# Performance work log

Measured on AMD Instinct MI355X. Metric: run time of the kernel, lower is better.

The kernel has to match this reference:

```python
import jax, jax.numpy as jnp
import numpy as np


def _spectral_normalize(W):
    # spectral_norm divides the weight by its largest singular value
    sigma = jnp.linalg.norm(W, ord=2)
    return W / sigma


def setup_inputs() -> dict:
    key = jax.random.key(0)
    ks = jax.random.split(key, 8)
    B, C, H, W = 2, 64, 96, 96
    C8 = C // 8
    x = jax.random.normal(ks[0], (B, C, H, W), dtype=jnp.float32)
    Wq = jax.random.normal(ks[1], (C8, C), dtype=jnp.float32) * 0.1
    bq = jax.random.normal(ks[2], (C8,), dtype=jnp.float32) * 0.1
    Wk = jax.random.normal(ks[3], (C8, C), dtype=jnp.float32) * 0.1
    bk = jax.random.normal(ks[4], (C8,), dtype=jnp.float32) * 0.1
    Wv = jax.random.normal(ks[5], (C, C), dtype=jnp.float32) * 0.1
    bv = jax.random.normal(ks[6], (C,), dtype=jnp.float32) * 0.1
    gamma = jnp.ones((1,), dtype=jnp.float32)
    return {"x": x, "Wq": Wq, "bq": bq, "Wk": Wk, "bk": bk,
            "Wv": Wv, "bv": bv, "gamma": gamma}


def reference(x, Wq, bq, Wk, bk, Wv, bv, gamma):
    B, C, H, W = x.shape
    xf = x.reshape(B, C, H * W)                       # [B, C, N]
    Wq_n = _spectral_normalize(Wq)
    Wk_n = _spectral_normalize(Wk)
    Wv_n = _spectral_normalize(Wv)
    # 1x1 Conv1d == matmul over channel dim
    f = jnp.einsum('oc,bcn->bon', Wq_n, xf) + bq[None, :, None]   # [B, C/8, N]
    g = jnp.einsum('oc,bcn->bon', Wk_n, xf) + bk[None, :, None]   # [B, C/8, N]
    h = jnp.einsum('oc,bcn->bon', Wv_n, xf) + bv[None, :, None]   # [B, C, N]
    # scores[b,i,j] = sum_c f[b,c,i] * g[b,c,j];  softmax over dim=1 (i)
    scores = jnp.einsum('bci,bcj->bij', f, g)                      # [B, N, N]
    beta = jax.nn.softmax(scores, axis=1)
    # o[b,c,j] = sum_i h[b,c,i] * beta[b,i,j]
    o = gamma[0] * jnp.einsum('bci,bij->bcj', h, beta) + xf
    return o.reshape(B, C, H, W)
```

## Files before the change

### kernel.cpp

```cpp
#include <hip/hip_runtime.h>


#define N_PIX 9216
#define N_B   2
#define N_C   64

typedef _Float16 half8  __attribute__((ext_vector_type(8)));
typedef _Float16 half4v __attribute__((ext_vector_type(4)));
typedef float    float4v __attribute__((ext_vector_type(4)));

#define LOG2E 1.44269504088896340736f
#define EXP_SHIFT 12.0f

__global__ __launch_bounds__(64) void k_sigma(const float* __restrict__ Wq,
                                              const float* __restrict__ Wk,
                                              const float* __restrict__ Wv,
                                              float* __restrict__ sig) {
  __shared__ float G8[8][8];
  __shared__ float Wl[64 * 64];
  __shared__ _Float16 Wh[64 * 80];
  __shared__ _Float16 Gh[64 * 80];
  const int t = threadIdx.x;
  const int mat = blockIdx.x;
  if (mat < 2) {
    const float* W = (mat == 0) ? Wq : Wk;
    const int i = t >> 3, j = t & 7;
    float g = 0.f;
    for (int c = 0; c < 64; ++c) g += W[i * 64 + c] * W[j * 64 + c];
    G8[i][j] = g;
    __syncthreads();
    const int L = t & 7;
    float G0[8], Gr[8];
    for (int k = 0; k < 8; ++k) { G0[k] = G8[L][k]; Gr[k] = G0[k]; }
    for (int it = 0; it < 8; ++it) {
      float g2[8] = {0, 0, 0, 0, 0, 0, 0, 0};
      for (int k = 0; k < 8; ++k) {
        float gik = Gr[k];
        for (int jj = 0; jj < 8; ++jj) g2[jj] += gik * __shfl(Gr[jj], k, 64);
      }
      float mx = 0.f;
      for (int jj = 0; jj < 8; ++jj) mx = fmaxf(mx, fabsf(g2[jj]));
      for (int d = 1; d < 8; d <<= 1) mx = fmaxf(mx, __shfl_xor(mx, d, 64));
      float r = 1.f / mx;
      for (int jj = 0; jj < 8; ++jj) Gr[jj] = g2[jj] * r;
    }
    float u = 0.f;
    for (int jj = 0; jj < 8; ++jj) u += Gr[jj];
    float y = 0.f;
    for (int k = 0; k < 8; ++k) y += G0[k] * __shfl(u, k, 64);
    float nu = u * y, de = u * u;
    for (int d = 1; d < 8; d <<= 1) { nu += __shfl_xor(nu, d, 64); de += __shfl_xor(de, d, 64); }
    if (t == 0) sig[mat] = sqrtf(nu / de);
  } else {
    for (int idx = t; idx < 4096; idx += 64) Wl[idx] = Wv[idx];
    __syncthreads();
    for (int idx = t; idx < 4096; idx += 64) Wh[(idx >> 6) * 80 + (idx & 63)] = (_Float16)Wl[idx];
    __syncthreads();
    const int lane15 = t & 15, quad = t >> 4;
    half8 fr[4][2];
    for (int rb = 0; rb < 4; ++rb)
      for (int kc = 0; kc < 2; ++kc)
        fr[rb][kc] = *(const half8*)&Wh[(lane15 + 16 * rb) * 80 + 32 * kc + 8 * quad];
    float4v D[4][4];
    for (int mb = 0; mb < 4; ++mb) for (int nb = 0; nb < 4; ++nb) D[mb][nb] = (float4v){0.f, 0.f, 0.f, 0.f};
    for (int kc = 0; kc < 2; ++kc)
      for (int mb = 0; mb < 4; ++mb)
        for (int nb = 0; nb < 4; ++nb)
          D[mb][nb] = __builtin_amdgcn_mfma_f32_16x16x32_f16(fr[mb][kc], fr[nb][kc], D[mb][nb], 0, 0, 0);
    for (int it = 0; it < 8; ++it) {
      float mx = 0.f;
      for (int mb = 0; mb < 4; ++mb) for (int nb = 0; nb < 4; ++nb) for (int r = 0; r < 4; ++r)
        mx = fmaxf(mx, fabsf(D[mb][nb][r]));
      for (int d = 1; d < 64; d <<= 1) mx = fmaxf(mx, __shfl_xor(mx, d, 64));
      float rs = 1.f / mx;
      for (int mb = 0; mb < 4; ++mb) for (int nb = 0; nb < 4; ++nb) for (int r = 0; r < 4; ++r)
        Gh[(4 * quad + r + 16 * mb) * 80 + lane15 + 16 * nb] = (_Float16)(D[mb][nb][r] * rs);
      __syncthreads();
      if (it == 7) break;
      for (int rb = 0; rb < 4; ++rb)
        for (int kc = 0; kc < 2; ++kc)
          fr[rb][kc] = *(const half8*)&Gh[(lane15 + 16 * rb) * 80 + 32 * kc + 8 * quad];
      for (int mb = 0; mb < 4; ++mb) for (int nb = 0; nb < 4; ++nb) D[mb][nb] = (float4v){0.f, 0.f, 0.f, 0.f};
      for (int kc = 0; kc < 2; ++kc)
        for (int mb = 0; mb < 4; ++mb)
          for (int nb = 0; nb < 4; ++nb)
            D[mb][nb] = __builtin_amdgcn_mfma_f32_16x16x32_f16(fr[mb][kc], fr[nb][kc], D[mb][nb], 0, 0, 0);
      __syncthreads();
    }
    float u = 0.f;
    for (int c = 0; c < 64; ++c) u += (float)Gh[t * 80 + c];
    float z = 0.f;
    for (int i2 = 0; i2 < 64; ++i2) z += Wl[i2 * 64 + t] * __shfl(u, i2, 64);
    float nu = z * z, de = u * u;
    for (int d = 1; d < 64; d <<= 1) { nu += __shfl_xor(nu, d, 64); de += __shfl_xor(de, d, 64); }
    if (t == 0) sig[2] = sqrtf(nu / de);
  }
}

__global__ __launch_bounds__(128) void k_wconv(const float* __restrict__ Wq, const float* __restrict__ bq,
                                               const float* __restrict__ Wk, const float* __restrict__ bk,
                                               const float* __restrict__ Wv, const float* __restrict__ bv,
                                               const float* __restrict__ sig,
                                               _Float16* __restrict__ W16, float* __restrict__ b80,
                                               unsigned* __restrict__ maxKu) {
  const float iq = LOG2E / sig[0], ik = 1.0f / sig[1], iv = 1.0f / sig[2];
  const int t = threadIdx.x;
  for (int idx = t; idx < 80 * 64; idx += 128) {
    const int m = idx >> 6, c = idx & 63;
    float v;
    if (m < 8)       v = Wq[m * 64 + c] * iq;
    else if (m < 16) v = Wk[(m - 8) * 64 + c] * ik;
    else             v = Wv[(m - 16) * 64 + c] * iv;
    W16[idx] = (_Float16)v;
  }
  if (t < 80) {
    float v;
    if (t < 8)       v = bq[t] * LOG2E;
    else if (t < 16) v = bk[t - 8];
    else             v = bv[t - 16];
    b80[t] = v;
  }
  if (t < 2) maxKu[t] = 0u;
}

__global__ __launch_bounds__(256) void k_fgh(const float* __restrict__ x,
                                             const _Float16* __restrict__ W16,
                                             const float* __restrict__ b80,
                                             _Float16* __restrict__ K16,
                                             _Float16* __restrict__ Q16,
                                             _Float16* __restrict__ VT16,
                                             unsigned* __restrict__ maxKu) {
  const int wave = threadIdx.x >> 6;
  const int lane = threadIdx.x & 63;
  const int lane15 = lane & 15, quad = lane >> 4;
  const int tile = blockIdx.x * 4 + wave;
  const int b = tile / 576;
  const int n = (tile % 576) * 16 + lane15;
  half8 wf[5][2];
  for (int mb = 0; mb < 5; ++mb)
    for (int kc = 0; kc < 2; ++kc)
      wf[mb][kc] = *(const half8*)&W16[(lane15 + 16 * mb) * 64 + 32 * kc + 8 * quad];
  float4v acc[5];
  for (int mb = 0; mb < 5; ++mb) acc[mb] = *(const float4v*)&b80[16 * mb + 4 * quad];
  const float* xb = x + (size_t)b * N_C * N_PIX;
  for (int kc = 0; kc < 2; ++kc) {
    half8 bf;
    for (int j = 0; j < 8; ++j)
      bf[j] = (_Float16)xb[(size_t)(32 * kc + 8 * quad + j) * N_PIX + n];
    for (int mb = 0; mb < 5; ++mb)
      acc[mb] = __builtin_amdgcn_mfma_f32_16x16x32_f16(wf[mb][kc], bf, acc[mb], 0, 0, 0);
  }
  {
    _Float16* dstK = K16 + ((size_t)b * N_PIX + n) * 8;
    _Float16* dstQ = Q16 + ((size_t)b * N_PIX + n) * 8;
    for (int r = 0; r < 4; ++r) {
      const int m = 4 * quad + r;
      const _Float16 v = (_Float16)acc[0][r];
      if (m < 8) dstK[m] = v; else dstQ[m - 8] = v;
    }
  }
  for (int mb = 1; mb < 5; ++mb)
    for (int r = 0; r < 4; ++r) {
      const int c = 4 * quad + r + 16 * (mb - 1);
      VT16[((size_t)b * N_C + c) * N_PIX + n] = (_Float16)acc[mb][r];
    }
  float sq = 0.f;
  if (quad < 2)
    for (int r = 0; r < 4; ++r) sq += acc[0][r] * acc[0][r];
  sq += __shfl_xor(sq, 16, 64);
  for (int d = 1; d < 64; d <<= 1) sq = fmaxf(sq, __shfl_xor(sq, d, 64));
  if (lane == 0) atomicMax(&maxKu[b], __float_as_uint(sq));
}


__device__ __forceinline__ void gload16(const _Float16* g, _Float16* l) {
  __builtin_amdgcn_global_load_lds(
      (const __attribute__((address_space(1))) void*)g,
      (__attribute__((address_space(3))) void*)l, 16, 0, 0);
}

__global__ __launch_bounds__(256, 2) void k_attn(const _Float16* __restrict__ K16,
                                                 const _Float16* __restrict__ Q16,
                                                 const _Float16* __restrict__ VT16,
                                                 const unsigned* __restrict__ maxKu,
                                                 const float* __restrict__ x,
                                                 const float* __restrict__ gamma,
                                                 float* __restrict__ out) {
  __shared__ __align__(16) _Float16 Vld[2][64 * 64];
  __shared__ __align__(16) _Float16 Pld[2][32 * 72];
  __shared__ float Lsh[4][32];
  const int wave = threadIdx.x >> 6;
  const int lane = threadIdx.x & 63;
  const int lane15 = lane & 15, quad = lane >> 4;
  const int tile = blockIdx.x;
  const int b = tile / 288;
  const int jb = (tile % 288) * 32;
  const float gm = gamma[0];
  const _Float16* Kb = K16 + (size_t)b * N_PIX * 8;
  const _Float16* Vb = VT16 + (size_t)b * N_C * N_PIX;
  const int srow = lane >> 3;
  const int scol = (lane & 7) ^ srow;
  const _Float16* gV0 = Vb + (size_t)(16 * wave + srow) * N_PIX + scol * 8;
  const _Float16* gV1 = Vb + (size_t)(16 * wave + 8 + srow) * N_PIX + scol * 8;

  half8 qf0 = {}, qf1 = {};
  if (quad == 0) {
    qf0 = *(const half8*)(Q16 + ((size_t)b * N_PIX + jb + lane15) * 8);
    qf1 = *(const half8*)(Q16 + ((size_t)b * N_PIX + jb + 16 + lane15) * 8);
  }
  const float maxK = sqrtf(__uint_as_float(maxKu[b]));
  float nq0 = 0.f, nq1 = 0.f;
  if (quad == 0)
#pragma unroll
    for (int j = 0; j < 8; ++j) {
      nq0 += (float)qf0[j] * (float)qf0[j];
      nq1 += (float)qf1[j] * (float)qf1[j];
    }
  nq0 = __shfl(nq0, lane15, 64);
  nq1 = __shfl(nq1, lane15, 64);
  const float M0 = sqrtf(nq0) * maxK - EXP_SHIFT;
  const float M1 = sqrtf(nq1) * maxK - EXP_SHIFT;

  float4v acc0 = {0.f, 0.f, 0.f, 0.f}, acc1 = {0.f, 0.f, 0.f, 0.f};
  float ls0 = 0.f, ls1 = 0.f;
  half8 kA = {}, kB = {};

  gload16(gV0, &Vld[0][(16 * wave) * 64]);
  gload16(gV1, &Vld[0][(16 * wave + 8) * 64]);
  if (quad == 0) kA = *(const half8*)(Kb + (size_t)(16 * wave + lane15) * 8);

  const float4v f4z = {0.f, 0.f, 0.f, 0.f};
#define ROUND(I0, BUF, KF, KN, PREF)                                                       \
  {                                                                                        \
    const int i1 = (I0) + 64;                                                              \
    if (PREF) {                                                                            \
      gload16(gV0 + i1, &Vld[BUF ^ 1][(16 * wave) * 64]);                                  \
      gload16(gV1 + i1, &Vld[BUF ^ 1][(16 * wave + 8) * 64]);                              \
      if (quad == 0) KN = *(const half8*)(Kb + (size_t)(i1 + 16 * wave + lane15) * 8);     \
    }                                                                                      \
    float4v s0 = __builtin_amdgcn_mfma_f32_16x16x32_f16(KF, qf0, f4z, 0, 0, 0);            \
    float4v s1 = __builtin_amdgcn_mfma_f32_16x16x32_f16(KF, qf1, f4z, 0, 0, 0);            \
    half4v h0, h1;                                                                         \
    _Pragma("unroll") for (int r = 0; r < 4; ++r) {                                        \
      const float p0 = __builtin_amdgcn_exp2f(s0[r] - M0);                                 \
      const float p1 = __builtin_amdgcn_exp2f(s1[r] - M1);                                 \
      h0[r] = (_Float16)p0; ls0 += (float)h0[r];                                           \
      h1[r] = (_Float16)p1; ls1 += (float)h1[r];                                           \
    }                                                                                      \
    *(half4v*)&Pld[BUF][lane15 * 72 + 16 * wave + 4 * quad] = h0;                          \
    *(half4v*)&Pld[BUF][(16 + lane15) * 72 + 16 * wave + 4 * quad] = h1;                   \
    __syncthreads();                                                                       \
    const half8 pf00 = *(const half8*)&Pld[BUF][lane15 * 72 + 8 * quad];                   \
    const half8 pf01 = *(const half8*)&Pld[BUF][lane15 * 72 + 32 + 8 * quad];              \
    const half8 pf10 = *(const half8*)&Pld[BUF][(16 + lane15) * 72 + 8 * quad];            \
    const half8 pf11 = *(const half8*)&Pld[BUF][(16 + lane15) * 72 + 32 + 8 * quad];       \
    const half8 vf0 = *(const half8*)&Vld[BUF][(16 * wave + lane15) * 64 +                 \
                                              ((quad ^ (lane15 & 7)) << 3)];               \
    const half8 vf1 = *(const half8*)&Vld[BUF][(16 * wave + lane15) * 64 +                 \
                                              (((4 + quad) ^ (lane15 & 7)) << 3)];         \
    acc0 = __builtin_amdgcn_mfma_f32_16x16x32_f16(pf00, vf0, acc0, 0, 0, 0);               \
    acc0 = __builtin_amdgcn_mfma_f32_16x16x32_f16(pf01, vf1, acc0, 0, 0, 0);               \
    acc1 = __builtin_amdgcn_mfma_f32_16x16x32_f16(pf10, vf0, acc1, 0, 0, 0);               \
    acc1 = __builtin_amdgcn_mfma_f32_16x16x32_f16(pf11, vf1, acc1, 0, 0, 0);               \
  }

#pragma unroll 1
  for (int r2 = 0; r2 < N_PIX / 128; ++r2) {
    const int i0 = r2 * 128;
    ROUND(i0, 0, kA, kB, true)
    ROUND(i0 + 64, 1, kB, kA, (i0 + 128) < N_PIX)
  }
#undef ROUND

  ls0 += __shfl_xor(ls0, 16, 64); ls0 += __shfl_xor(ls0, 32, 64);
  ls1 += __shfl_xor(ls1, 16, 64); ls1 += __shfl_xor(ls1, 32, 64);
  if (quad == 0) { Lsh[wave][lane15] = ls0; Lsh[wave][16 + lane15] = ls1; }
  __syncthreads();
  float4v lt0 = {0.f, 0.f, 0.f, 0.f}, lt1 = {0.f, 0.f, 0.f, 0.f};
#pragma unroll
  for (int w = 0; w < 4; ++w) {
    const float4v a = *(const float4v*)&Lsh[w][4 * quad];
    const float4v c = *(const float4v*)&Lsh[w][16 + 4 * quad];
#pragma unroll
    for (int r = 0; r < 4; ++r) { lt0[r] += a[r]; lt1[r] += c[r]; }
  }
  const int ch = 16 * wave + lane15;
  const float* xb = x + (size_t)b * N_C * N_PIX;
  float* ob = out + (size_t)b * N_C * N_PIX;
  {
    const size_t idx = (size_t)ch * N_PIX + jb + 4 * quad;
    const float4v xr = *(const float4v*)(xb + idx);
    float4v o;
#pragma unroll
    for (int r = 0; r < 4; ++r) o[r] = gm * acc0[r] / lt0[r] + xr[r];
    *(float4v*)(ob + idx) = o;
  }
  {
    const size_t idx = (size_t)ch * N_PIX + jb + 16 + 4 * quad;
    const float4v xr = *(const float4v*)(xb + idx);
    float4v o;
#pragma unroll
    for (int r = 0; r < 4; ++r) o[r] = gm * acc1[r] / lt1[r] + xr[r];
    *(float4v*)(ob + idx) = o;
  }
}

extern "C" void kernel_launch(void* const* d_in, const int* in_sizes, int n_in,
                              void* d_out, int out_size, void* d_ws, size_t ws_size,
                              hipStream_t stream) {
  const float* x     = (const float*)d_in[0];
  const float* Wq    = (const float*)d_in[1];
  const float* bq    = (const float*)d_in[2];
  const float* Wk    = (const float*)d_in[3];
  const float* bk    = (const float*)d_in[4];
  const float* Wv    = (const float*)d_in[5];
  const float* bv    = (const float*)d_in[6];
  const float* gamma = (const float*)d_in[7];
  float* out = (float*)d_out;

  char* ws = (char*)d_ws;
  float*    sig   = (float*)ws;
  unsigned* maxKu = (unsigned*)(ws + 16);
  float*    b80   = (float*)(ws + 32);
  _Float16* W16   = (_Float16*)(ws + 512);
  _Float16* K16   = (_Float16*)(ws + 10752);
  _Float16* Q16   = (_Float16*)(ws + 10752 + 294912);
  _Float16* VT16  = (_Float16*)(ws + 10752 + 2 * 294912);

  hipLaunchKernelGGL(k_sigma, dim3(3), dim3(64), 0, stream, Wq, Wk, Wv, sig);
  hipLaunchKernelGGL(k_wconv, dim3(1), dim3(128), 0, stream, Wq, bq, Wk, bk, Wv, bv, sig, W16, b80, maxKu);
  hipLaunchKernelGGL(k_fgh, dim3(288), dim3(256), 0, stream, x, W16, b80, K16, Q16, VT16, maxKu);
  hipLaunchKernelGGL(k_attn, dim3(576), dim3(256), 0, stream, K16, Q16, VT16, maxKu, x, gamma, out);
}
```

Measured before the change: 200.8 us.

## Split key range across waves with private P tiles and final cross-wave reduction

Each wave now handles its own interleaved slice of the key/pixel dimension and computes all 64 output channels for the 32 query columns. This removes the per-round __syncthreads and the shared V staging. V fragments are loaded straight from global memory into registers, double-buffered in registers. Partial outputs are reduced across the four waves through a new shared Osh buffer at the end. The trade-off is higher register pressure (eight accumulators plus eight V fragments) and uncoalesced 16-byte global V loads per lane, with no LDS reuse of V across waves.

```diff
diff --git a/kernel.cpp b/kernel.cpp
--- a/kernel.cpp
+++ b/kernel.cpp
@@ -173,12 +173,6 @@
 }
 
 
-__device__ __forceinline__ void gload16(const _Float16* g, _Float16* l) {
-  __builtin_amdgcn_global_load_lds(
-      (const __attribute__((address_space(1))) void*)g,
-      (__attribute__((address_space(3))) void*)l, 16, 0, 0);
-}
-
 __global__ __launch_bounds__(256, 2) void k_attn(const _Float16* __restrict__ K16,
                                                  const _Float16* __restrict__ Q16,
                                                  const _Float16* __restrict__ VT16,
@@ -186,9 +180,9 @@
                                                  const float* __restrict__ x,
                                                  const float* __restrict__ gamma,
                                                  float* __restrict__ out) {
-  __shared__ __align__(16) _Float16 Vld[2][64 * 64];
-  __shared__ __align__(16) _Float16 Pld[2][32 * 72];
+  __shared__ __align__(16) _Float16 P_lds[4][32 * 40];
   __shared__ float Lsh[4][32];
+  __shared__ float Osh[4][64][33];
   const int wave = threadIdx.x >> 6;
   const int lane = threadIdx.x & 63;
   const int lane15 = lane & 15, quad = lane >> 4;
@@ -198,10 +192,11 @@
   const float gm = gamma[0];
   const _Float16* Kb = K16 + (size_t)b * N_PIX * 8;
   const _Float16* Vb = VT16 + (size_t)b * N_C * N_PIX;
-  const int srow = lane >> 3;
-  const int scol = (lane & 7) ^ srow;
-  const _Float16* gV0 = Vb + (size_t)(16 * wave + srow) * N_PIX + scol * 8;
-  const _Float16* gV1 = Vb + (size_t)(16 * wave + 8 + srow) * N_PIX + scol * 8;
+  _Float16* Pl = P_lds[wave];
+  const _Float16* pV0 = Vb + (size_t)(lane15) * N_PIX + 8 * quad;
+  const _Float16* pV1 = Vb + (size_t)(lane15 + 16) * N_PIX + 8 * quad;
+  const _Float16* pV2 = Vb + (size_t)(lane15 + 32) * N_PIX + 8 * quad;
+  const _Float16* pV3 = Vb + (size_t)(lane15 + 48) * N_PIX + 8 * quad;
 
   half8 qf0 = {}, qf1 = {};
   if (quad == 0) {
@@ -221,60 +216,87 @@
   const float M0 = sqrtf(nq0) * maxK - EXP_SHIFT;
   const float M1 = sqrtf(nq1) * maxK - EXP_SHIFT;
 
-  float4v acc0 = {0.f, 0.f, 0.f, 0.f}, acc1 = {0.f, 0.f, 0.f, 0.f};
+  float4v a00 = {0.f,0.f,0.f,0.f}, a01 = {0.f,0.f,0.f,0.f}, a02 = {0.f,0.f,0.f,0.f}, a03 = {0.f,0.f,0.f,0.f};
+  float4v a10 = {0.f,0.f,0.f,0.f}, a11 = {0.f,0.f,0.f,0.f}, a12 = {0.f,0.f,0.f,0.f}, a13 = {0.f,0.f,0.f,0.f};
   float ls0 = 0.f, ls1 = 0.f;
-  half8 kA = {}, kB = {};
-
-  gload16(gV0, &Vld[0][(16 * wave) * 64]);
-  gload16(gV1, &Vld[0][(16 * wave + 8) * 64]);
-  if (quad == 0) kA = *(const half8*)(Kb + (size_t)(16 * wave + lane15) * 8);
-
   const float4v f4z = {0.f, 0.f, 0.f, 0.f};
-#define ROUND(I0, BUF, KF, KN, PREF)                                                       \
-  {                                                                                        \
-    const int i1 = (I0) + 64;                                                              \
-    if (PREF) {                                                                            \
-      gload16(gV0 + i1, &Vld[BUF ^ 1][(16 * wave) * 64]);                                  \
-      gload16(gV1 + i1, &Vld[BUF ^ 1][(16 * wave + 8) * 64]);                              \
-      if (quad == 0) KN = *(const half8*)(Kb + (size_t)(i1 + 16 * wave + lane15) * 8);     \
-    }                                                                                      \
-    float4v s0 = __builtin_amdgcn_mfma_f32_16x16x32_f16(KF, qf0, f4z, 0, 0, 0);            \
-    float4v s1 = __builtin_amdgcn_mfma_f32_16x16x32_f16(KF, qf1, f4z, 0, 0, 0);            \
-    half4v h0, h1;                                                                         \
-    _Pragma("unroll") for (int r = 0; r < 4; ++r) {                                        \
-      const float p0 = __builtin_amdgcn_exp2f(s0[r] - M0);                                 \
-      const float p1 = __builtin_amdgcn_exp2f(s1[r] - M1);                                 \
-      h0[r] = (_Float16)p0; ls0 += (float)h0[r];                                           \
-      h1[r] = (_Float16)p1; ls1 += (float)h1[r];                                           \
-    }                                                                                      \
-    *(half4v*)&Pld[BUF][lane15 * 72 + 16 * wave + 4 * quad] = h0;                          \
-    *(half4v*)&Pld[BUF][(16 + lane15) * 72 + 16 * wave + 4 * quad] = h1;                   \
-    __syncthreads();                                                                       \
-    const half8 pf00 = *(const half8*)&Pld[BUF][lane15 * 72 + 8 * quad];                   \
-    const half8 pf01 = *(const half8*)&Pld[BUF][lane15 * 72 + 32 + 8 * quad];              \
-    const half8 pf10 = *(const half8*)&Pld[BUF][(16 + lane15) * 72 + 8 * quad];            \
-    const half8 pf11 = *(const half8*)&Pld[BUF][(16 + lane15) * 72 + 32 + 8 * quad];       \
-    const half8 vf0 = *(const half8*)&Vld[BUF][(16 * wave + lane15) * 64 +                 \
-                                              ((quad ^ (lane15 & 7)) << 3)];               \
-    const half8 vf1 = *(const half8*)&Vld[BUF][(16 * wave + lane15) * 64 +                 \
-                                              (((4 + quad) ^ (lane15 & 7)) << 3)];         \
-    acc0 = __builtin_amdgcn_mfma_f32_16x16x32_f16(pf00, vf0, acc0, 0, 0, 0);               \
-    acc0 = __builtin_amdgcn_mfma_f32_16x16x32_f16(pf01, vf1, acc0, 0, 0, 0);               \
-    acc1 = __builtin_amdgcn_mfma_f32_16x16x32_f16(pf10, vf0, acc1, 0, 0, 0);               \
-    acc1 = __builtin_amdgcn_mfma_f32_16x16x32_f16(pf11, vf1, acc1, 0, 0, 0);               \
+
+  half8 kA0 = {}, kA1 = {}, kB0 = {}, kB1 = {};
+  half8 vA0, vA1, vA2, vA3, vB0, vB1, vB2, vB3;
+
+#define LOADK(K0, K1, I)                                                \
+  if (quad == 0) {                                                      \
+    K0 = *(const half8*)(Kb + (size_t)((I) + lane15) * 8);              \
+    K1 = *(const half8*)(Kb + (size_t)((I) + 16 + lane15) * 8);         \
+  }
+#define LOADV(V0, V1, V2, V3, I)                                        \
+  V0 = *(const half8*)(pV0 + (I));                                      \
+  V1 = *(const half8*)(pV1 + (I));                                      \
+  V2 = *(const half8*)(pV2 + (I));                                      \
+  V3 = *(const half8*)(pV3 + (I));
+
+  const int base = 32 * wave;
+  LOADK(kA0, kA1, base)
+  LOADV(vA0, vA1, vA2, vA3, base)
+
+#define ROUND(KF0, KF1, VF0, VF1, VF2, VF3, KN0, KN1, VN0, VN1, VN2, VN3, PI, PREF) \
+  {                                                                                 \
+    if (PREF) { LOADK(KN0, KN1, PI) LOADV(VN0, VN1, VN2, VN3, PI) }                 \
+    float4v s00 = __builtin_amdgcn_mfma_f32_16x16x32_f16(KF0, qf0, f4z, 0, 0, 0);   \
+    float4v s01 = __builtin_amdgcn_mfma_f32_16x16x32_f16(KF0, qf1, f4z, 0, 0, 0);   \
+    float4v s10 = __builtin_amdgcn_mfma_f32_16x16x32_f16(KF1, qf0, f4z, 0, 0, 0);   \
+    float4v s11 = __builtin_amdgcn_mfma_f32_16x16x32_f16(KF1, qf1, f4z, 0, 0, 0);   \
+    half4v h00, h01, h10, h11;                                                      \
+    _Pragma("unroll") for (int r = 0; r < 4; ++r) {                                 \
+      const float p00 = __builtin_amdgcn_exp2f(s00[r] - M0);                        \
+      const float p01 = __builtin_amdgcn_exp2f(s01[r] - M1);                        \
+      const float p10 = __builtin_amdgcn_exp2f(s10[r] - M0);                        \
+      const float p11 = __builtin_amdgcn_exp2f(s11[r] - M1);                        \
+      h00[r] = (_Float16)p00; ls0 += (float)h00[r];                                 \
+      h01[r] = (_Float16)p01; ls1 += (float)h01[r];                                 \
+      h10[r] = (_Float16)p10; ls0 += (float)h10[r];                                 \
+      h11[r] = (_Float16)p11; ls1 += (float)h11[r];                                 \
+    }                                                                               \
+    *(half4v*)&Pl[lane15 * 40 + 4 * quad] = h00;                                    \
+    *(half4v*)&Pl[lane15 * 40 + 16 + 4 * quad] = h10;                               \
+    *(half4v*)&Pl[(16 + lane15) * 40 + 4 * quad] = h01;                             \
+    *(half4v*)&Pl[(16 + lane15) * 40 + 16 + 4 * quad] = h11;                        \
+    const half8 pf0 = *(const half8*)&Pl[lane15 * 40 + 8 * quad];                   \
+    const half8 pf1 = *(const half8*)&Pl[(16 + lane15) * 40 + 8 * quad];            \
+    a00 = __builtin_amdgcn_mfma_f32_16x16x32_f16(pf0, VF0, a00, 0, 0, 0);           \
+    a01 = __builtin_amdgcn_mfma_f32_16x16x32_f16(pf0, VF1, a01, 0, 0, 0);           \
+    a02 = __builtin_amdgcn_mfma_f32_16x16x32_f16(pf0, VF2, a02, 0, 0, 0);           \
+    a03 = __builtin_amdgcn_mfma_f32_16x16x32_f16(pf0, VF3, a03, 0, 0, 0);           \
+    a10 = __builtin_amdgcn_mfma_f32_16x16x32_f16(pf1, VF0, a10, 0, 0, 0);           \
+    a11 = __builtin_amdgcn_mfma_f32_16x16x32_f16(pf1, VF1, a11, 0, 0, 0);           \
+    a12 = __builtin_amdgcn_mfma_f32_16x16x32_f16(pf1, VF2, a12, 0, 0, 0);           \
+    a13 = __builtin_amdgcn_mfma_f32_16x16x32_f16(pf1, VF3, a13, 0, 0, 0);           \
   }
 
 #pragma unroll 1
-  for (int r2 = 0; r2 < N_PIX / 128; ++r2) {
-    const int i0 = r2 * 128;
-    ROUND(i0, 0, kA, kB, true)
-    ROUND(i0 + 64, 1, kB, kA, (i0 + 128) < N_PIX)
+  for (int j = 0; j < 36; ++j) {
+    const int i0 = 256 * j + base;
+    ROUND(kA0, kA1, vA0, vA1, vA2, vA3, kB0, kB1, vB0, vB1, vB2, vB3, i0 + 128, true)
+    ROUND(kB0, kB1, vB0, vB1, vB2, vB3, kA0, kA1, vA0, vA1, vA2, vA3, i0 + 256, j < 35)
   }
 #undef ROUND
+#undef LOADK
+#undef LOADV
 
   ls0 += __shfl_xor(ls0, 16, 64); ls0 += __shfl_xor(ls0, 32, 64);
   ls1 += __shfl_xor(ls1, 16, 64); ls1 += __shfl_xor(ls1, 32, 64);
   if (quad == 0) { Lsh[wave][lane15] = ls0; Lsh[wave][16 + lane15] = ls1; }
+#pragma unroll
+  for (int r = 0; r < 4; ++r) {
+    Osh[wave][lane][r]      = a00[r];
+    Osh[wave][lane][4 + r]  = a01[r];
+    Osh[wave][lane][8 + r]  = a02[r];
+    Osh[wave][lane][12 + r] = a03[r];
+    Osh[wave][lane][16 + r] = a10[r];
+    Osh[wave][lane][20 + r] = a11[r];
+    Osh[wave][lane][24 + r] = a12[r];
+    Osh[wave][lane][28 + r] = a13[r];
+  }
   __syncthreads();
   float4v lt0 = {0.f, 0.f, 0.f, 0.f}, lt1 = {0.f, 0.f, 0.f, 0.f};
 #pragma unroll
@@ -284,6 +306,14 @@
 #pragma unroll
     for (int r = 0; r < 4; ++r) { lt0[r] += a[r]; lt1[r] += c[r]; }
   }
+  float4v o0 = {0.f, 0.f, 0.f, 0.f}, o1 = {0.f, 0.f, 0.f, 0.f};
+#pragma unroll
+  for (int w = 0; w < 4; ++w)
+#pragma unroll
+    for (int r = 0; r < 4; ++r) {
+      o0[r] += Osh[w][lane][4 * wave + r];
+      o1[r] += Osh[w][lane][16 + 4 * wave + r];
+    }
   const int ch = 16 * wave + lane15;
   const float* xb = x + (size_t)b * N_C * N_PIX;
   float* ob = out + (size_t)b * N_C * N_PIX;
@@ -292,7 +322,7 @@
     const float4v xr = *(const float4v*)(xb + idx);
     float4v o;
 #pragma unroll
-    for (int r = 0; r < 4; ++r) o[r] = gm * acc0[r] / lt0[r] + xr[r];
+    for (int r = 0; r < 4; ++r) o[r] = gm * o0[r] / lt0[r] + xr[r];
     *(float4v*)(ob + idx) = o;
   }
   {
@@ -300,7 +330,7 @@
     const float4v xr = *(const float4v*)(xb + idx);
     float4v o;
 #pragma unroll
-    for (int r = 0; r < 4; ++r) o[r] = gm * acc1[r] / lt1[r] + xr[r];
+    for (int r = 0; r < 4; ++r) o[r] = gm * o1[r] / lt1[r] + xr[r];
     *(float4v*)(ob + idx) = o;
   }
 }
```

Measured after the change: 221.0 us. 10.0% more time.

## Split key range across waves to remove per-round block barriers in attention

Applied to the files above, without the earlier changes.

Each wave now handles its own 32-key slice per round for all 64 channels, keeping per-wave K/V/P tiles in LDS. This removes the __syncthreads per round. Partial output accumulators are reduced across waves through shared memory at the end. LDS reads and vmcnt waits use inline asm to control the pipelining. The cost is more accumulator registers (8 MFMA tiles) and an extra LDS reduction epilogue.

```diff
diff --git a/kernel.cpp b/kernel.cpp
--- a/kernel.cpp
+++ b/kernel.cpp
@@ -8,6 +8,7 @@
 typedef _Float16 half8  __attribute__((ext_vector_type(8)));
 typedef _Float16 half4v __attribute__((ext_vector_type(4)));
 typedef float    float4v __attribute__((ext_vector_type(4)));
+typedef int      int4v  __attribute__((ext_vector_type(4)));
 
 #define LOG2E 1.44269504088896340736f
 #define EXP_SHIFT 12.0f
@@ -179,6 +180,22 @@
       (__attribute__((address_space(3))) void*)l, 16, 0, 0);
 }
 
+#define VMWAIT5() asm volatile("s_waitcnt vmcnt(5)" ::: "memory")
+#define DS2(D0, D1, P0, P1)                                              \
+  asm volatile("ds_read_b128 %0, %2\n\t"                                 \
+               "ds_read_b128 %1, %3\n\t"                                 \
+               "s_waitcnt lgkmcnt(0)"                                    \
+               : "=&v"(D0), "=&v"(D1) : "v"(P0), "v"(P1) : "memory")
+#define DS4(D0, D1, D2, D3, P0, P1, P2, P3)                              \
+  asm volatile("ds_read_b128 %0, %4\n\t"                                 \
+               "ds_read_b128 %1, %5\n\t"                                 \
+               "ds_read_b128 %2, %6\n\t"                                 \
+               "ds_read_b128 %3, %7\n\t"                                 \
+               "s_waitcnt lgkmcnt(0)"                                    \
+               : "=&v"(D0), "=&v"(D1), "=&v"(D2), "=&v"(D3)              \
+               : "v"(P0), "v"(P1), "v"(P2), "v"(P3) : "memory")
+typedef const __attribute__((address_space(3))) _Float16* lds_cp;
+
 __global__ __launch_bounds__(256, 2) void k_attn(const _Float16* __restrict__ K16,
                                                  const _Float16* __restrict__ Q16,
                                                  const _Float16* __restrict__ VT16,
@@ -186,9 +203,11 @@
                                                  const float* __restrict__ x,
                                                  const float* __restrict__ gamma,
                                                  float* __restrict__ out) {
-  __shared__ __align__(16) _Float16 Vld[2][64 * 64];
-  __shared__ __align__(16) _Float16 Pld[2][32 * 72];
+  __shared__ __align__(16) _Float16 Kld[2][4][64 * 8];
+  __shared__ __align__(16) _Float16 Vld[2][4][64 * 32];
+  __shared__ __align__(16) _Float16 Pld[4][32 * 40];
   __shared__ float Lsh[4][32];
+  __shared__ float Osh[4][64][17];
   const int wave = threadIdx.x >> 6;
   const int lane = threadIdx.x & 63;
   const int lane15 = lane & 15, quad = lane >> 4;
@@ -198,10 +217,7 @@
   const float gm = gamma[0];
   const _Float16* Kb = K16 + (size_t)b * N_PIX * 8;
   const _Float16* Vb = VT16 + (size_t)b * N_C * N_PIX;
-  const int srow = lane >> 3;
-  const int scol = (lane & 7) ^ srow;
-  const _Float16* gV0 = Vb + (size_t)(16 * wave + srow) * N_PIX + scol * 8;
-  const _Float16* gV1 = Vb + (size_t)(16 * wave + 8 + srow) * N_PIX + scol * 8;
+  _Float16* Pl = Pld[wave];
 
   half8 qf0 = {}, qf1 = {};
   if (quad == 0) {
@@ -221,60 +237,93 @@
   const float M0 = sqrtf(nq0) * maxK - EXP_SHIFT;
   const float M1 = sqrtf(nq1) * maxK - EXP_SHIFT;
 
-  float4v acc0 = {0.f, 0.f, 0.f, 0.f}, acc1 = {0.f, 0.f, 0.f, 0.f};
+  float4v a00 = {0.f,0.f,0.f,0.f}, a01 = {0.f,0.f,0.f,0.f}, a02 = {0.f,0.f,0.f,0.f}, a03 = {0.f,0.f,0.f,0.f};
+  float4v a10 = {0.f,0.f,0.f,0.f}, a11 = {0.f,0.f,0.f,0.f}, a12 = {0.f,0.f,0.f,0.f}, a13 = {0.f,0.f,0.f,0.f};
   float ls0 = 0.f, ls1 = 0.f;
-  half8 kA = {}, kB = {};
-
-  gload16(gV0, &Vld[0][(16 * wave) * 64]);
-  gload16(gV1, &Vld[0][(16 * wave + 8) * 64]);
-  if (quad == 0) kA = *(const half8*)(Kb + (size_t)(16 * wave + lane15) * 8);
-
   const float4v f4z = {0.f, 0.f, 0.f, 0.f};
-#define ROUND(I0, BUF, KF, KN, PREF)                                                       \
-  {                                                                                        \
-    const int i1 = (I0) + 64;                                                              \
-    if (PREF) {                                                                            \
-      gload16(gV0 + i1, &Vld[BUF ^ 1][(16 * wave) * 64]);                                  \
-      gload16(gV1 + i1, &Vld[BUF ^ 1][(16 * wave + 8) * 64]);                              \
-      if (quad == 0) KN = *(const half8*)(Kb + (size_t)(i1 + 16 * wave + lane15) * 8);     \
-    }                                                                                      \
-    float4v s0 = __builtin_amdgcn_mfma_f32_16x16x32_f16(KF, qf0, f4z, 0, 0, 0);            \
-    float4v s1 = __builtin_amdgcn_mfma_f32_16x16x32_f16(KF, qf1, f4z, 0, 0, 0);            \
-    half4v h0, h1;                                                                         \
-    _Pragma("unroll") for (int r = 0; r < 4; ++r) {                                        \
-      const float p0 = __builtin_amdgcn_exp2f(s0[r] - M0);                                 \
-      const float p1 = __builtin_amdgcn_exp2f(s1[r] - M1);                                 \
-      h0[r] = (_Float16)p0; ls0 += (float)h0[r];                                           \
-      h1[r] = (_Float16)p1; ls1 += (float)h1[r];                                           \
-    }                                                                                      \
-    *(half4v*)&Pld[BUF][lane15 * 72 + 16 * wave + 4 * quad] = h0;                          \
-    *(half4v*)&Pld[BUF][(16 + lane15) * 72 + 16 * wave + 4 * quad] = h1;                   \
-    __syncthreads();                                                                       \
-    const half8 pf00 = *(const half8*)&Pld[BUF][lane15 * 72 + 8 * quad];                   \
-    const half8 pf01 = *(const half8*)&Pld[BUF][lane15 * 72 + 32 + 8 * quad];              \
-    const half8 pf10 = *(const half8*)&Pld[BUF][(16 + lane15) * 72 + 8 * quad];            \
-    const half8 pf11 = *(const half8*)&Pld[BUF][(16 + lane15) * 72 + 32 + 8 * quad];       \
-    const half8 vf0 = *(const half8*)&Vld[BUF][(16 * wave + lane15) * 64 +                 \
-                                              ((quad ^ (lane15 & 7)) << 3)];               \
-    const half8 vf1 = *(const half8*)&Vld[BUF][(16 * wave + lane15) * 64 +                 \
-                                              (((4 + quad) ^ (lane15 & 7)) << 3)];         \
-    acc0 = __builtin_amdgcn_mfma_f32_16x16x32_f16(pf00, vf0, acc0, 0, 0, 0);               \
-    acc0 = __builtin_amdgcn_mfma_f32_16x16x32_f16(pf01, vf1, acc0, 0, 0, 0);               \
-    acc1 = __builtin_amdgcn_mfma_f32_16x16x32_f16(pf10, vf0, acc1, 0, 0, 0);               \
-    acc1 = __builtin_amdgcn_mfma_f32_16x16x32_f16(pf11, vf1, acc1, 0, 0, 0);               \
-  }
+
+#define STAGE(SLOT, I0)                                                          \
+  {                                                                              \
+    const int _i = (I0);                                                         \
+    gload16(Kb + (size_t)(_i + (lane & 31)) * 8, &Kld[SLOT][wave][0]);           \
+    gload16(Vb + (size_t)(lane >> 2) * N_PIX + _i + (lane & 3) * 8,              \
+            &Vld[SLOT][wave][0]);                                                \
+    gload16(Vb + (size_t)(16 + (lane >> 2)) * N_PIX + _i + (lane & 3) * 8,       \
+            &Vld[SLOT][wave][512]);                                              \
+    gload16(Vb + (size_t)(32 + (lane >> 2)) * N_PIX + _i + (lane & 3) * 8,       \
+            &Vld[SLOT][wave][1024]);                                             \
+    gload16(Vb + (size_t)(48 + (lane >> 2)) * N_PIX + _i + (lane & 3) * 8,       \
+            &Vld[SLOT][wave][1536]);                                             \
+  }
+
+  STAGE(0, 32 * wave)
 
 #pragma unroll 1
-  for (int r2 = 0; r2 < N_PIX / 128; ++r2) {
-    const int i0 = r2 * 128;
-    ROUND(i0, 0, kA, kB, true)
-    ROUND(i0 + 64, 1, kB, kA, (i0 + 128) < N_PIX)
-  }
-#undef ROUND
+  for (int r = 0; r < 72; ++r) {
+    const int slot = r & 1, nslot = slot ^ 1;
+    const int i1 = (r < 71) ? (128 * (r + 1) + 32 * wave) : (128 * 71 + 32 * wave);
+    STAGE(nslot, i1)
+    VMWAIT5();
+    int4v k0i, k1i;
+    {
+      lds_cp pk0 = (lds_cp)&Kld[slot][wave][lane15 * 8];
+      lds_cp pk1 = (lds_cp)&Kld[slot][wave][(16 + lane15) * 8];
+      DS2(k0i, k1i, pk0, pk1);
+    }
+    const half8 kf0 = __builtin_bit_cast(half8, k0i);
+    const half8 kf1 = __builtin_bit_cast(half8, k1i);
+    float4v s00 = __builtin_amdgcn_mfma_f32_16x16x32_f16(kf0, qf0, f4z, 0, 0, 0);
+    float4v s10 = __builtin_amdgcn_mfma_f32_16x16x32_f16(kf1, qf0, f4z, 0, 0, 0);
+    float4v s01 = __builtin_amdgcn_mfma_f32_16x16x32_f16(kf0, qf1, f4z, 0, 0, 0);
+    float4v s11 = __builtin_amdgcn_mfma_f32_16x16x32_f16(kf1, qf1, f4z, 0, 0, 0);
+    half4v h00, h10, h01, h11;
+#pragma unroll
+    for (int rr = 0; rr < 4; ++rr) {
+      const float p00 = __builtin_amdgcn_exp2f(s00[rr] - M0);
+      const float p10 = __builtin_amdgcn_exp2f(s10[rr] - M0);
+      const float p01 = __builtin_amdgcn_exp2f(s01[rr] - M1);
+      const float p11 = __builtin_amdgcn_exp2f(s11[rr] - M1);
+      h00[rr] = (_Float16)p00; ls0 += (float)h00[rr];
+      h10[rr] = (_Float16)p10; ls0 += (float)h10[rr];
+      h01[rr] = (_Float16)p01; ls1 += (float)h01[rr];
+      h11[rr] = (_Float16)p11; ls1 += (float)h11[rr];
+    }
+    *(half4v*)&Pl[lane15 * 40 + 4 * quad] = h00;
+    *(half4v*)&Pl[lane15 * 40 + 16 + 4 * quad] = h10;
+    *(half4v*)&Pl[(16 + lane15) * 40 + 4 * quad] = h01;
+    *(half4v*)&Pl[(16 + lane15) * 40 + 16 + 4 * quad] = h11;
+    const half8 pf0 = *(const half8*)&Pl[lane15 * 40 + 8 * quad];
+    const half8 pf1 = *(const half8*)&Pl[(16 + lane15) * 40 + 8 * quad];
+    int4v v0i, v1i, v2i, v3i;
+    {
+      lds_cp pv0 = (lds_cp)&Vld[slot][wave][lane15 * 32 + 8 * quad];
+      lds_cp pv1 = (lds_cp)&Vld[slot][wave][512 + lane15 * 32 + 8 * quad];
+      lds_cp pv2 = (lds_cp)&Vld[slot][wave][1024 + lane15 * 32 + 8 * quad];
+      lds_cp pv3 = (lds_cp)&Vld[slot][wave][1536 + lane15 * 32 + 8 * quad];
+      DS4(v0i, v1i, v2i, v3i, pv0, pv1, pv2, pv3);
+    }
+    a00 = __builtin_amdgcn_mfma_f32_16x16x32_f16(pf0, __builtin_bit_cast(half8, v0i), a00, 0, 0, 0);
+    a01 = __builtin_amdgcn_mfma_f32_16x16x32_f16(pf0, __builtin_bit_cast(half8, v1i), a01, 0, 0, 0);
+    a02 = __builtin_amdgcn_mfma_f32_16x16x32_f16(pf0, __builtin_bit_cast(half8, v2i), a02, 0, 0, 0);
+    a03 = __builtin_amdgcn_mfma_f32_16x16x32_f16(pf0, __builtin_bit_cast(half8, v3i), a03, 0, 0, 0);
+    a10 = __builtin_amdgcn_mfma_f32_16x16x32_f16(pf1, __builtin_bit_cast(half8, v0i), a10, 0, 0, 0);
+    a11 = __builtin_amdgcn_mfma_f32_16x16x32_f16(pf1, __builtin_bit_cast(half8, v1i), a11, 0, 0, 0);
+    a12 = __builtin_amdgcn_mfma_f32_16x16x32_f16(pf1, __builtin_bit_cast(half8, v2i), a12, 0, 0, 0);
+    a13 = __builtin_amdgcn_mfma_f32_16x16x32_f16(pf1, __builtin_bit_cast(half8, v3i), a13, 0, 0, 0);
+  }
+#undef STAGE
+  asm volatile("s_waitcnt vmcnt(0)" ::: "memory");
 
   ls0 += __shfl_xor(ls0, 16, 64); ls0 += __shfl_xor(ls0, 32, 64);
   ls1 += __shfl_xor(ls1, 16, 64); ls1 += __shfl_xor(ls1, 32, 64);
   if (quad == 0) { Lsh[wave][lane15] = ls0; Lsh[wave][16 + lane15] = ls1; }
+#pragma unroll
+  for (int rr = 0; rr < 4; ++rr) {
+    Osh[wave][lane][rr]      = a00[rr];
+    Osh[wave][lane][4 + rr]  = a01[rr];
+    Osh[wave][lane][8 + rr]  = a02[rr];
+    Osh[wave][lane][12 + rr] = a03[rr];
+  }
   __syncthreads();
   float4v lt0 = {0.f, 0.f, 0.f, 0.f}, lt1 = {0.f, 0.f, 0.f, 0.f};
 #pragma unroll
@@ -282,25 +331,44 @@
     const float4v a = *(const float4v*)&Lsh[w][4 * quad];
     const float4v c = *(const float4v*)&Lsh[w][16 + 4 * quad];
 #pragma unroll
-    for (int r = 0; r < 4; ++r) { lt0[r] += a[r]; lt1[r] += c[r]; }
+    for (int rr = 0; rr < 4; ++rr) { lt0[rr] += a[rr]; lt1[rr] += c[rr]; }
   }
   const int ch = 16 * wave + lane15;
   const float* xb = x + (size_t)b * N_C * N_PIX;
   float* ob = out + (size_t)b * N_C * N_PIX;
   {
+    float4v osum = {0.f, 0.f, 0.f, 0.f};
+#pragma unroll
+    for (int w = 0; w < 4; ++w)
+#pragma unroll
+      for (int rr = 0; rr < 4; ++rr) osum[rr] += Osh[w][lane][4 * wave + rr];
     const size_t idx = (size_t)ch * N_PIX + jb + 4 * quad;
     const float4v xr = *(const float4v*)(xb + idx);
     float4v o;
 #pragma unroll
-    for (int r = 0; r < 4; ++r) o[r] = gm * acc0[r] / lt0[r] + xr[r];
+    for (int rr = 0; rr < 4; ++rr) o[rr] = gm * osum[rr] / lt0[rr] + xr[rr];
     *(float4v*)(ob + idx) = o;
   }
+  __syncthreads();
+#pragma unroll
+  for (int rr = 0; rr < 4; ++rr) {
+    Osh[wave][lane][rr]      = a10[rr];
+    Osh[wave][lane][4 + rr]  = a11[rr];
+    Osh[wave][lane][8 + rr]  = a12[rr];
+    Osh[wave][lane][12 + rr] = a13[rr];
+  }
+  __syncthreads();
   {
+    float4v osum = {0.f, 0.f, 0.f, 0.f};
+#pragma unroll
+    for (int w = 0; w < 4; ++w)
+#pragma unroll
+      for (int rr = 0; rr < 4; ++rr) osum[rr] += Osh[w][lane][4 * wave + rr];
     const size_t idx = (size_t)ch * N_PIX + jb + 16 + 4 * quad;
     const float4v xr = *(const float4v*)(xb + idx);
     float4v o;
 #pragma unroll
-    for (int r = 0; r < 4; ++r) o[r] = gm * acc1[r] / lt1[r] + xr[r];
+    for (int rr = 0; rr < 4; ++rr) o[rr] = gm * osum[rr] / lt1[rr] + xr[rr];
     *(float4v*)(ob + idx) = o;
   }
 }
```

After: 198.0 us. Within noise of the previous version (-1.4%).
